# Optimization experiments

Hardware: AMD Instinct MI355X
Metric: run time of the kernel (lower is better)

Reference implementation:

```python
import jax, jax.numpy as jnp
import numpy as np

BATCH, CLASSES = 32768, 1000
SMOOTHING = 0.1  # timm-style LabelSmoothingCrossEntropy default


def setup_inputs() -> dict:
    key = jax.random.key(0)
    k1, k2 = jax.random.split(key)
    output = jax.random.normal(k1, (BATCH, CLASSES), dtype=jnp.float32)
    target = jax.random.randint(k2, (BATCH,), 0, CLASSES, dtype=jnp.int64)
    return {"output": output, "target": target}


def _label_smoothing_ce(x, target, smoothing=SMOOTHING):
    # timm-style: loss = (1-eps)*NLL + eps*mean(-logp)
    logp = jax.nn.log_softmax(x, axis=-1)
    nll = -jnp.take_along_axis(logp, target[:, None], axis=-1)[:, 0]
    smooth = -logp.mean(axis=-1)
    return ((1.0 - smoothing) * nll + smoothing * smooth).mean()


def reference(output, target):
    batch, classes = output.shape
    probs = jax.nn.softmax(output, axis=1)  # [B, C]
    # per-class empirical frequency via one-pass bincount
    counts = jnp.zeros((classes,), dtype=probs.dtype).at[target].add(1.0)
    avg_count = counts / batch                 # [C]
    avg_conf = probs.mean(axis=0)              # [C]
    loss_mdca = jnp.abs(avg_conf - avg_count).sum() / classes
    # faithful to original: label-smoothing CE applied to softmaxed output
    loss_ce = _label_smoothing_ce(probs, target)
    loss = loss_ce + loss_mdca
    return (loss, loss_ce, loss_mdca)
```

## Files before the change

### kernel.cpp

```cpp
#include <hip/hip_runtime.h>
#include <math.h>

#define BATCH   32768
#define CLASSES 1000
#define C4      (CLASSES / 4)
#define EPS     0.1f
#define LOG1001 6.9087547794f

#define MB   2048
#define MT   256
#define WPB  4
#define NPROC (MB * WPB)
#define RPW   (BATCH / NPROC)

#define PSTRIDE   2048
#define PARTIAL_F 0
#define STAGE2_F  (MB * PSTRIDE)

__global__ __launch_bounds__(MT, 4)
void mdca_main(const float* __restrict__ x, const int* __restrict__ target,
               float* __restrict__ partial) {
    __shared__ float cs[WPB][1024];
    __shared__ float cnt[1024];
    __shared__ float red[2][WPB];

    const int tid  = threadIdx.x;
    const int wave = tid >> 6;
    const int lane = tid & 63;

    float4* my4 = reinterpret_cast<float4*>(cs[wave]);
    #pragma unroll
    for (int k = 0; k < 4; ++k) my4[64 * k + lane] = make_float4(0.f, 0.f, 0.f, 0.f);
    #pragma unroll
    for (int c = tid; c < 1024; c += MT) cnt[c] = 0.f;
    __syncthreads();

    const int proc = blockIdx.x * WPB + wave;
    const int r0   = proc * RPW;

    int t[RPW];
    #pragma unroll
    for (int s = 0; s < RPW; ++s) t[s] = target[r0 + s];

    const float4* base4 = reinterpret_cast<const float4*>(x + (size_t)r0 * CLASSES);
    float4 v[RPW][4];
    #pragma unroll
    for (int s = 0; s < RPW; ++s) {
        #pragma unroll
        for (int k = 0; k < 4; ++k) {
            const int idx4 = 64 * k + lane;
            v[s][k] = (idx4 < C4) ? base4[s * C4 + idx4]
                                  : make_float4(-INFINITY, -INFINITY, -INFINITY, -INFINITY);
        }
    }

    float z[RPW], et[RPW];
    #pragma unroll
    for (int s = 0; s < RPW; ++s) {
        float zl = 0.f, el = 0.f;
        #pragma unroll
        for (int k = 0; k < 4; ++k) {
            float4 e;
            e.x = __expf(v[s][k].x); e.y = __expf(v[s][k].y);
            e.z = __expf(v[s][k].z); e.w = __expf(v[s][k].w);
            v[s][k] = e;
            zl += (e.x + e.y) + (e.z + e.w);
            const int d = t[s] - 4 * (64 * k + lane);
            if ((unsigned)d < 4u)
                el = (d == 0) ? e.x : (d == 1) ? e.y : (d == 2) ? e.z : e.w;
        }
        z[s] = zl; et[s] = el;
    }
    #pragma unroll
    for (int o = 32; o > 0; o >>= 1) {
        #pragma unroll
        for (int s = 0; s < RPW; ++s) z[s] += __shfl_xor(z[s], o, 64);
    }

    float iz[RPW];
    float q = 0.f, pa = 0.f;
    #pragma unroll
    for (int s = 0; s < RPW; ++s) {
        iz[s] = 1.0f / z[s];
        pa   += et[s] * iz[s];
    }

    #pragma unroll
    for (int k = 0; k < 4; ++k) {
        const int idx4 = 64 * k + lane;
        if (idx4 < C4) {
            float4 col = my4[idx4];
            #pragma unroll
            for (int s = 0; s < RPW; ++s) {
                const float px = v[s][k].x * iz[s]; col.x += px; q = fmaf(px, px, q);
                const float py = v[s][k].y * iz[s]; col.y += py; q = fmaf(py, py, q);
                const float pz = v[s][k].z * iz[s]; col.z += pz; q = fmaf(pz, pz, q);
                const float pw = v[s][k].w * iz[s]; col.w += pw; q = fmaf(pw, pw, q);
            }
            my4[idx4] = col;
        }
    }

    if (lane == 0) {
        #pragma unroll
        for (int s = 0; s < RPW; ++s) atomicAdd(&cnt[t[s]], 1.0f);
    }

    #pragma unroll
    for (int o = 32; o > 0; o >>= 1) {
        q  += __shfl_xor(q,  o, 64);
        pa += __shfl_xor(pa, o, 64);
    }
    if (lane == 0) { red[0][wave] = q; red[1][wave] = pa; }
    __syncthreads();

    float* ps = partial + (size_t)blockIdx.x * PSTRIDE;
    #pragma unroll
    for (int c = tid; c < 1024; c += MT) {
        if (c < 1000) {
            float s = 0.f;
            #pragma unroll
            for (int w = 0; w < WPB; ++w) s += cs[w][c];
            ps[c] = s;
        }
        ps[1024 + c] = cnt[c];
    }
    if (tid == 0) {
        float sq = 0.f, sp = 0.f;
        #pragma unroll
        for (int w = 0; w < WPB; ++w) { sq += red[0][w]; sp += red[1][w]; }
        ps[1000] = sq;
        ps[1001] = sp;
    }
}

__global__ __launch_bounds__(128)
void mdca_reduce(const float* __restrict__ partial, float* __restrict__ stage2) {
    const int bg = blockIdx.x >> 4;
    const int cg = blockIdx.x & 15;
    const int cc = cg * 128 + threadIdx.x;
    const int b0 = bg * (MB / 8);
    float a0 = 0.f, a1 = 0.f, a2 = 0.f, a3 = 0.f;
    for (int b = b0; b < b0 + MB / 8; b += 4) {
        a0 += partial[(size_t)(b + 0) * PSTRIDE + cc];
        a1 += partial[(size_t)(b + 1) * PSTRIDE + cc];
        a2 += partial[(size_t)(b + 2) * PSTRIDE + cc];
        a3 += partial[(size_t)(b + 3) * PSTRIDE + cc];
    }
    stage2[(size_t)bg * PSTRIDE + cc] = (a0 + a1) + (a2 + a3);
}

__global__ __launch_bounds__(1024)
void mdca_final(const float* __restrict__ stage2, float* __restrict__ out) {
    __shared__ float red[16];
    const int tid = threadIdx.x, wave = tid >> 6, lane = tid & 63;
    float d = 0.f;
    if (tid < CLASSES) {
        float conf = 0.f, c2 = 0.f;
        #pragma unroll
        for (int bg = 0; bg < 8; ++bg) {
            conf += stage2[bg * PSTRIDE + tid];
            c2   += stage2[bg * PSTRIDE + 1024 + tid];
        }
        d = fabsf(conf - c2) * (1.0f / BATCH);
    }
    #pragma unroll
    for (int o = 32; o > 0; o >>= 1) d += __shfl_xor(d, o, 64);
    if (lane == 0) red[wave] = d;
    __syncthreads();
    if (tid == 0) {
        float tot = 0.f;
        #pragma unroll
        for (int w = 0; w < 16; ++w) tot += red[w];
        float q = 0.f, pa = 0.f;
        #pragma unroll
        for (int bg = 0; bg < 8; ++bg) {
            q  += stage2[bg * PSTRIDE + 1000];
            pa += stage2[bg * PSTRIDE + 1001];
        }
        const float mdca = tot / CLASSES;
        const float ce = LOG1001 + 0.5f * q / (1001.0f * BATCH)
                       - (1.0f - EPS) * (pa * (1.0f / BATCH))
                       - EPS / CLASSES;
        out[0] = ce + mdca;
        out[1] = ce;
        out[2] = mdca;
    }
}

extern "C" void kernel_launch(void* const* d_in, const int* in_sizes, int n_in,
                              void* d_out, int out_size, void* d_ws, size_t ws_size,
                              hipStream_t stream) {
    const float* x   = (const float*)d_in[0];
    const int*   tgt = (const int*)d_in[1];
    float* out = (float*)d_out;
    float* ws  = (float*)d_ws;

    mdca_main<<<MB, MT, 0, stream>>>(x, tgt, ws + PARTIAL_F);
    mdca_reduce<<<128, 128, 0, stream>>>(ws + PARTIAL_F, ws + STAGE2_F);
    mdca_final<<<1, 1024, 0, stream>>>(ws + STAGE2_F, out);
}
```

Measured before the change: 218.8 us.

## Use fewer larger blocks with multi-pass strided rows per wave

```diff
diff --git a/kernel.cpp b/kernel.cpp
--- a/kernel.cpp
+++ b/kernel.cpp
@@ -7,11 +7,12 @@
 #define EPS     0.1f
 #define LOG1001 6.9087547794f
 
-#define MB   2048
-#define MT   256
-#define WPB  4
+#define MB    512
+#define MT    512
+#define WPB   8
 #define NPROC (MB * WPB)
-#define RPW   (BATCH / NPROC)
+#define ILP   4
+#define OUTER 2
 
 #define PSTRIDE   2048
 #define PARTIAL_F 0
@@ -31,79 +32,80 @@
     float4* my4 = reinterpret_cast<float4*>(cs[wave]);
     #pragma unroll
     for (int k = 0; k < 4; ++k) my4[64 * k + lane] = make_float4(0.f, 0.f, 0.f, 0.f);
-    #pragma unroll
-    for (int c = tid; c < 1024; c += MT) cnt[c] = 0.f;
+    cnt[tid] = 0.f; cnt[tid + 512] = 0.f;
     __syncthreads();
 
     const int proc = blockIdx.x * WPB + wave;
-    const int r0   = proc * RPW;
-
-    int t[RPW];
-    #pragma unroll
-    for (int s = 0; s < RPW; ++s) t[s] = target[r0 + s];
-
-    const float4* base4 = reinterpret_cast<const float4*>(x + (size_t)r0 * CLASSES);
-    float4 v[RPW][4];
-    #pragma unroll
-    for (int s = 0; s < RPW; ++s) {
+    float q = 0.f, pa = 0.f;
+
+    #pragma unroll
+    for (int outer = 0; outer < OUTER; ++outer) {
+        int t[ILP];
+        float4 v[ILP][4];
+        #pragma unroll
+        for (int s = 0; s < ILP; ++s) t[s] = target[proc + (outer * ILP + s) * NPROC];
+        #pragma unroll
+        for (int s = 0; s < ILP; ++s) {
+            const int r = proc + (outer * ILP + s) * NPROC;
+            const float4* row4 = reinterpret_cast<const float4*>(x + (size_t)r * CLASSES);
+            #pragma unroll
+            for (int k = 0; k < 4; ++k) {
+                const int idx4 = 64 * k + lane;
+                v[s][k] = (idx4 < C4) ? row4[idx4]
+                                      : make_float4(-INFINITY, -INFINITY, -INFINITY, -INFINITY);
+            }
+        }
+
+        float z[ILP], et[ILP];
+        #pragma unroll
+        for (int s = 0; s < ILP; ++s) {
+            float zl = 0.f, el = 0.f;
+            #pragma unroll
+            for (int k = 0; k < 4; ++k) {
+                float4 e;
+                e.x = __expf(v[s][k].x); e.y = __expf(v[s][k].y);
+                e.z = __expf(v[s][k].z); e.w = __expf(v[s][k].w);
+                v[s][k] = e;
+                zl += (e.x + e.y) + (e.z + e.w);
+                const int d = t[s] - 4 * (64 * k + lane);
+                if ((unsigned)d < 4u)
+                    el = (d == 0) ? e.x : (d == 1) ? e.y : (d == 2) ? e.z : e.w;
+            }
+            z[s] = zl; et[s] = el;
+        }
+        #pragma unroll
+        for (int o = 32; o > 0; o >>= 1) {
+            #pragma unroll
+            for (int s = 0; s < ILP; ++s) z[s] += __shfl_xor(z[s], o, 64);
+        }
+
+        float iz[ILP];
+        #pragma unroll
+        for (int s = 0; s < ILP; ++s) {
+            iz[s] = 1.0f / z[s];
+            pa   += et[s] * iz[s];
+        }
+
         #pragma unroll
         for (int k = 0; k < 4; ++k) {
             const int idx4 = 64 * k + lane;
-            v[s][k] = (idx4 < C4) ? base4[s * C4 + idx4]
-                                  : make_float4(-INFINITY, -INFINITY, -INFINITY, -INFINITY);
-        }
-    }
-
-    float z[RPW], et[RPW];
-    #pragma unroll
-    for (int s = 0; s < RPW; ++s) {
-        float zl = 0.f, el = 0.f;
-        #pragma unroll
-        for (int k = 0; k < 4; ++k) {
-            float4 e;
-            e.x = __expf(v[s][k].x); e.y = __expf(v[s][k].y);
-            e.z = __expf(v[s][k].z); e.w = __expf(v[s][k].w);
-            v[s][k] = e;
-            zl += (e.x + e.y) + (e.z + e.w);
-            const int d = t[s] - 4 * (64 * k + lane);
-            if ((unsigned)d < 4u)
-                el = (d == 0) ? e.x : (d == 1) ? e.y : (d == 2) ? e.z : e.w;
-        }
-        z[s] = zl; et[s] = el;
-    }
-    #pragma unroll
-    for (int o = 32; o > 0; o >>= 1) {
-        #pragma unroll
-        for (int s = 0; s < RPW; ++s) z[s] += __shfl_xor(z[s], o, 64);
-    }
-
-    float iz[RPW];
-    float q = 0.f, pa = 0.f;
-    #pragma unroll
-    for (int s = 0; s < RPW; ++s) {
-        iz[s] = 1.0f / z[s];
-        pa   += et[s] * iz[s];
-    }
-
-    #pragma unroll
-    for (int k = 0; k < 4; ++k) {
-        const int idx4 = 64 * k + lane;
-        if (idx4 < C4) {
-            float4 col = my4[idx4];
-            #pragma unroll
-            for (int s = 0; s < RPW; ++s) {
-                const float px = v[s][k].x * iz[s]; col.x += px; q = fmaf(px, px, q);
-                const float py = v[s][k].y * iz[s]; col.y += py; q = fmaf(py, py, q);
-                const float pz = v[s][k].z * iz[s]; col.z += pz; q = fmaf(pz, pz, q);
-                const float pw = v[s][k].w * iz[s]; col.w += pw; q = fmaf(pw, pw, q);
+            if (idx4 < C4) {
+                float4 col = my4[idx4];
+                #pragma unroll
+                for (int s = 0; s < ILP; ++s) {
+                    const float px = v[s][k].x * iz[s]; col.x += px; q = fmaf(px, px, q);
+                    const float py = v[s][k].y * iz[s]; col.y += py; q = fmaf(py, py, q);
+                    const float pz = v[s][k].z * iz[s]; col.z += pz; q = fmaf(pz, pz, q);
+                    const float pw = v[s][k].w * iz[s]; col.w += pw; q = fmaf(pw, pw, q);
+                }
+                my4[idx4] = col;
             }
-            my4[idx4] = col;
-        }
-    }
-
-    if (lane == 0) {
-        #pragma unroll
-        for (int s = 0; s < RPW; ++s) atomicAdd(&cnt[t[s]], 1.0f);
+        }
+
+        if (lane == 0) {
+            #pragma unroll
+            for (int s = 0; s < ILP; ++s) atomicAdd(&cnt[t[s]], 1.0f);
+        }
     }
 
     #pragma unroll
```

Result: faster. 200.8 us (median of 2 runs) (-8.2%).
